# Kernel tuning notes

Measured on AMD Instinct MI355X. Metric: run time of the kernel, lower is better.

## Reference

```python
import jax, jax.numpy as jnp
import numpy as np

B, T, D, H = 2, 2048, 1024, 16
HS = D // H
EPS = 1e-5


def setup_inputs() -> dict:
    key = jax.random.key(0)
    ks = jax.random.split(key, 16)
    s = lambda *shape: 0.02
    inp = {
        "x": jax.random.normal(ks[0], (B, T, D), jnp.float32),
        # per-head Q/K/V weights stacked over heads: [H, D, HS]
        "Wq": jax.random.normal(ks[1], (H, D, HS), jnp.float32) * 0.02,
        "bq": jnp.zeros((H, HS), jnp.float32),
        "Wk": jax.random.normal(ks[2], (H, D, HS), jnp.float32) * 0.02,
        "bk": jnp.zeros((H, HS), jnp.float32),
        "Wv": jax.random.normal(ks[3], (H, D, HS), jnp.float32) * 0.02,
        "bv": jnp.zeros((H, HS), jnp.float32),
        "Wp": jax.random.normal(ks[4], (D, D), jnp.float32) * 0.02,
        "bp": jnp.zeros((D,), jnp.float32),
        "W1": jax.random.normal(ks[5], (D, 4 * D), jnp.float32) * 0.02,
        "b1": jnp.zeros((4 * D,), jnp.float32),
        "W2": jax.random.normal(ks[6], (4 * D, D), jnp.float32) * 0.02,
        "b2": jnp.zeros((D,), jnp.float32),
        "g1": jnp.ones((D,), jnp.float32),
        "be1": jnp.zeros((D,), jnp.float32),
        "g2": jnp.ones((D,), jnp.float32),
        "be2": jnp.zeros((D,), jnp.float32),
    }
    return inp


def layernorm(x, g, b):
    mu = jnp.mean(x, axis=-1, keepdims=True)
    var = jnp.mean(jnp.square(x - mu), axis=-1, keepdims=True)
    return (x - mu) * jax.lax.rsqrt(var + EPS) * g + b


def reference(x, Wq, bq, Wk, bk, Wv, bv, Wp, bp, W1, b1, W2, b2, g1, be1, g2, be2):
    # NOTE: this block applies LN then residual-adds the *normalized* x,
    # exactly as in the original (x = ln1(x); x = x + mha(x)).
    h = layernorm(x, g1, be1)
    # multi-head attention, all heads batched via stacked weights
    q = jnp.einsum('btd,hdk->bhtk', h, Wq) + bq[None, :, None, :]
    k = jnp.einsum('btd,hdk->bhtk', h, Wk) + bk[None, :, None, :]
    v = jnp.einsum('btd,hdk->bhtk', h, Wv) + bv[None, :, None, :]
    att = jnp.einsum('bhtk,bhsk->bhts', q, k) * (HS ** -0.5)  # [B,H,T,T]
    att = jax.nn.softmax(att, axis=-1)
    o = jnp.einsum('bhts,bhsk->bhtk', att, v)  # [B,H,T,HS]
    # concat heads in order along last dim -> [B,T,D]
    o = jnp.transpose(o, (0, 2, 1, 3)).reshape(B, T, D)
    o = o @ Wp + bp
    h = h + o
    h2 = layernorm(h, g2, be2)
    ff = jax.nn.gelu(h2 @ W1 + b1, approximate=False) @ W2 + b2
    return h2 + ff
```

## Files before the change

kernel.cpp:

```cpp
#include <hip/hip_runtime.h>
#include <cstdint>
#include <cstddef>

#define B_  2
#define T_  2048
#define D_  1024
#define H_  16
#define HS_ 64
#define MTOT (B_*T_)

typedef unsigned short u16;
typedef __attribute__((ext_vector_type(8))) __bf16 bf16x8;
typedef __attribute__((ext_vector_type(4))) float f32x4;

__device__ __forceinline__ u16 f2bf(float f) {
  unsigned int u = __builtin_bit_cast(unsigned int, f);
  u += 0x7fffu + ((u >> 16) & 1u);
  return (u16)(u >> 16);
}

__device__ __forceinline__ unsigned cvtpk(float lo, float hi) {
  unsigned r;
  asm("v_cvt_pk_bf16_f32 %0, %1, %2" : "=v"(r) : "v"(lo), "v"(hi));
  return r;
}

__device__ __forceinline__ void gload16(const u16* g, u16* l) {
  __builtin_amdgcn_global_load_lds((const __attribute__((address_space(1))) void*)g,
                                   (__attribute__((address_space(3))) void*)l, 16, 0, 0);
}

__global__ __launch_bounds__(256) void transpose_f2b(const float* __restrict__ in,
                                                     u16* __restrict__ out, int R, int C) {
  __shared__ float tile[32][33];
  int c0 = blockIdx.x * 32, r0 = blockIdx.y * 32;
  size_t zoff = (size_t)blockIdx.z * R * C;
  const float* src = in + zoff;
  u16* dst = out + zoff;
  int tx = threadIdx.x & 31, ty = threadIdx.x >> 5;
#pragma unroll
  for (int k = 0; k < 4; ++k)
    tile[ty + k*8][tx] = src[(size_t)(r0 + ty + k*8) * C + c0 + tx];
  __syncthreads();
#pragma unroll
  for (int k = 0; k < 4; ++k)
    dst[(size_t)(c0 + ty + k*8) * R + r0 + tx] = f2bf(tile[tx][ty + k*8]);
}

__global__ __launch_bounds__(256) void transpose_v(const u16* __restrict__ in,
                                                   u16* __restrict__ out) {
  __shared__ u16 tile[32][33];
  int z = blockIdx.z;
  int b = z >> 4, h = z & 15;
  int t0 = blockIdx.x * 32, f0 = blockIdx.y * 32;
  int tx = threadIdx.x & 31, ty = threadIdx.x >> 5;
#pragma unroll
  for (int k = 0; k < 4; ++k)
    tile[ty + k*8][tx] = in[((size_t)b*T_ + t0 + ty + k*8) * D_ + h*HS_ + f0 + tx];
  __syncthreads();
#pragma unroll
  for (int k = 0; k < 4; ++k)
    out[((size_t)z*HS_ + f0 + ty + k*8) * T_ + t0 + tx] = tile[tx][ty + k*8];
}

__global__ __launch_bounds__(256) void ln_kernel(const float* __restrict__ x,
                                                 const float* __restrict__ gg,
                                                 const float* __restrict__ be,
                                                 float* __restrict__ hf,
                                                 u16* __restrict__ hb) {
  int row = blockIdx.x;
  int t = threadIdx.x;
  const float* xr = x + (size_t)row * D_;
  float4 xv = *(const float4*)&xr[t * 4];
  float s  = xv.x + xv.y + xv.z + xv.w;
  float ss = xv.x*xv.x + xv.y*xv.y + xv.z*xv.z + xv.w*xv.w;
#pragma unroll
  for (int m = 1; m < 64; m <<= 1) { s += __shfl_xor(s, m); ss += __shfl_xor(ss, m); }
  __shared__ float red[8];
  int lane = t & 63, wv = t >> 6;
  if (lane == 0) { red[wv] = s; red[4 + wv] = ss; }
  __syncthreads();
  s  = red[0] + red[1] + red[2] + red[3];
  ss = red[4] + red[5] + red[6] + red[7];
  float mu  = s * (1.0f / D_);
  float var = ss * (1.0f / D_) - mu * mu;
  float rs  = rsqrtf(var + 1e-5f);
  float4 gv = *(const float4*)&gg[t * 4];
  float4 bv = *(const float4*)&be[t * 4];
  float4 hv;
  hv.x = (xv.x - mu) * rs * gv.x + bv.x;
  hv.y = (xv.y - mu) * rs * gv.y + bv.y;
  hv.z = (xv.z - mu) * rs * gv.z + bv.z;
  hv.w = (xv.w - mu) * rs * gv.w + bv.w;
  *(float4*)&hf[(size_t)row * D_ + t * 4] = hv;
  uint2 pk;
  pk.x = (unsigned)f2bf(hv.x) | ((unsigned)f2bf(hv.y) << 16);
  pk.y = (unsigned)f2bf(hv.z) | ((unsigned)f2bf(hv.w) << 16);
  *(uint2*)&hb[(size_t)row * D_ + t * 4] = pk;
}

template<int EPI>
__global__ __launch_bounds__(256) void gemm_bt(
    const u16* __restrict__ A, const u16* __restrict__ Bt,
    const float* __restrict__ bias0, const float* __restrict__ bias1,
    const float* __restrict__ bias2, const float* __restrict__ res,
    float* __restrict__ outf, u16* __restrict__ o0, u16* __restrict__ o1,
    u16* __restrict__ o2, int M, int N, int K, int kLen) {
  __shared__ __align__(16) u16 As[3][128 * 32];
  __shared__ __align__(16) u16 Bs[3][128 * 32];
  const int tid = threadIdx.x;
  const int lane = tid & 63, wv = tid >> 6;
  const int m0 = blockIdx.y * 128, n0 = blockIdx.x * 128;
  const int kOff = blockIdx.z * kLen;
  const int rA = lane & 15, g = lane >> 4;
  const int wm = (wv >> 1) * 64, wn = (wv & 1) * 64;
  const int sx = (rA >> 1) & 3;

  f32x4 acc[4][4] = {};

  auto stage = [&](int tt, int bufi) {
#pragma unroll
    for (int p = 0; p < 2; ++p) {
      int c = (p * 4 + wv) * 64 + lane;
      int row = c >> 2;
      int s = (c & 3) ^ ((row >> 1) & 3);
      gload16(A  + (size_t)(m0 + row) * K + kOff + tt * 32 + s * 8,
              &As[bufi][0] + (size_t)(p * 4 + wv) * 512);
      gload16(Bt + (size_t)(n0 + row) * K + kOff + tt * 32 + s * 8,
              &Bs[bufi][0] + (size_t)(p * 4 + wv) * 512);
    }
  };

  const int nk = kLen >> 5;
  stage(0, 0);
  stage(1, 1);

  int cur = 0, nxt = 2;
  for (int t = 0; t < nk; ++t) {
    if (t + 1 < nk) asm volatile("s_waitcnt vmcnt(4)" ::: "memory");
    else            asm volatile("s_waitcnt vmcnt(0)" ::: "memory");
    __builtin_amdgcn_s_barrier();
    __builtin_amdgcn_sched_barrier(0);
    if (t + 2 < nk) stage(t + 2, nxt);

    bf16x8 a[4], b[4];
#pragma unroll
    for (int i = 0; i < 4; ++i)
      a[i] = *(const bf16x8*)&As[cur][(wm + i * 16 + rA) * 32 + ((g ^ sx) << 3)];
#pragma unroll
    for (int i = 0; i < 4; ++i)
      b[i] = *(const bf16x8*)&Bs[cur][(wn + i * 16 + rA) * 32 + ((g ^ sx) << 3)];
#pragma unroll
    for (int i = 0; i < 4; ++i)
#pragma unroll
      for (int j = 0; j < 4; ++j)
        acc[i][j] = __builtin_amdgcn_mfma_f32_16x16x32_bf16(a[i], b[j], acc[i][j], 0, 0, 0);

    cur = (cur == 2) ? 0 : cur + 1;
    nxt = (nxt == 2) ? 0 : nxt + 1;
  }

#pragma unroll
  for (int i = 0; i < 4; ++i) {
#pragma unroll
    for (int j = 0; j < 4; ++j) {
#pragma unroll
      for (int r = 0; r < 4; ++r) {
        int row = m0 + wm + i * 16 + g * 4 + r;
        int col = n0 + wn + j * 16 + rA;
        float v = acc[i][j][r];
        if constexpr (EPI == 0) {
          int sel = col >> 10, nn = col & 1023;
          const float* bp = sel == 0 ? bias0 : (sel == 1 ? bias1 : bias2);
          u16* op = sel == 0 ? o0 : (sel == 1 ? o1 : o2);
          op[(size_t)row * 1024 + nn] = f2bf(v + bp[nn]);
        } else if constexpr (EPI == 1) {
          v += bias0[col];
          float z = 0.7978845608f * (v + 0.044715f * v * v * v);
          z = fminf(z, 18.0f);
          float e = __builtin_amdgcn_exp2f(z * 2.8853900817779268f);
          v = v * e / (e + 1.0f);
          o0[(size_t)row * N + col] = f2bf(v);
        } else if constexpr (EPI == 2) {
          v += bias0[col] + res[(size_t)row * N + col];
          outf[(size_t)row * N + col] = v;
        } else {
          float* dst = blockIdx.z ? (float*)o1 : outf;
          dst[(size_t)row * N + col] = v;
        }
      }
    }
  }
}

__global__ __launch_bounds__(256) void reduce_ff2(const float* __restrict__ p0,
                                                  const float* __restrict__ p1,
                                                  const float* __restrict__ bias,
                                                  const float* __restrict__ res,
                                                  float* __restrict__ out) {
  int i = (blockIdx.x * 256 + threadIdx.x) * 4;
  float4 a = *(const float4*)&p0[i];
  float4 b = *(const float4*)&p1[i];
  float4 r = *(const float4*)&res[i];
  float4 bb = *(const float4*)&bias[i & 1023];
  float4 o;
  o.x = a.x + b.x + r.x + bb.x;
  o.y = a.y + b.y + r.y + bb.y;
  o.z = a.z + b.z + r.z + bb.z;
  o.w = a.w + b.w + r.w + bb.w;
  *(float4*)&out[i] = o;
}

__global__ __launch_bounds__(256) void attn_kernel(const u16* __restrict__ qg,
                                                   const u16* __restrict__ kg,
                                                   const u16* __restrict__ vtg,
                                                   u16* __restrict__ og) {
  const int wg = blockIdx.x;
  const int qt = wg & 31;
  const int h  = (wg >> 5) & 15;
  const int b  = wg >> 9;
  const int tid = threadIdx.x, lane = tid & 63, wv = tid >> 6;
  const int q0 = qt * 64 + wv * 16;
  const int rA = lane & 15, g = lane >> 4;
  const int rx = rA & 7;

  __shared__ __align__(16) u16 Ks[2][64 * 64];
  __shared__ __align__(16) u16 Vs[2][64 * 64];
  __shared__ __align__(16) u16 Ps[4][16 * 64];

  const size_t qoff = ((size_t)b * T_ + q0 + rA) * D_ + h * HS_ + g * 8;
  const bf16x8 aq0 = *(const bf16x8*)&qg[qoff];
  const bf16x8 aq1 = *(const bf16x8*)&qg[qoff + 32];

  const u16* kbase = kg + (size_t)b * T_ * D_ + h * HS_;
  const u16* vbase = vtg + ((size_t)b * H_ + h) * HS_ * T_;

  const float cfold = 0.18033688011112042f;
  float mrun = -1e30f, lrun = 0.0f;
  f32x4 oacc[4] = {};

  auto stage = [&](int t, int buf) {
#pragma unroll
    for (int p = 0; p < 2; ++p) {
      int chunk = p * 256 + wv * 64 + lane;
      int row = chunk >> 3, s = chunk & 7;
      int ss = s ^ (row & 7);
      gload16(kbase + ((size_t)t * 64 + row) * D_ + ss * 8,
              &Ks[buf][0] + (size_t)(p * 256 + wv * 64) * 8);
      gload16(vbase + (size_t)row * T_ + t * 64 + ss * 8,
              &Vs[buf][0] + (size_t)(p * 256 + wv * 64) * 8);
    }
  };

  stage(0, 0);

  const int NT = T_ / 64;
  for (int t = 0; t < NT; ++t) {
    __syncthreads();
    const int buf = t & 1;
    if (t + 1 < NT) stage(t + 1, buf ^ 1);

    const u16* kb = &Ks[buf][0];
    f32x4 sc[4];
    __builtin_amdgcn_s_setprio(1);
#pragma unroll
    for (int st = 0; st < 4; ++st) {
      bf16x8 k0 = *(const bf16x8*)&kb[(st * 16 + rA) * 64 + ((g ^ rx) << 3)];
      bf16x8 k1 = *(const bf16x8*)&kb[(st * 16 + rA) * 64 + (((4 + g) ^ rx) << 3)];
      f32x4 z = {};
      z = __builtin_amdgcn_mfma_f32_16x16x32_bf16(k0, aq0, z, 0, 0, 0);
      z = __builtin_amdgcn_mfma_f32_16x16x32_bf16(k1, aq1, z, 0, 0, 0);
      sc[st] = z;
    }
    __builtin_amdgcn_s_setprio(0);

    float a0 = fmaxf(fmaxf(sc[0][0], sc[0][1]), fmaxf(sc[0][2], sc[0][3]));
    float a1 = fmaxf(fmaxf(sc[1][0], sc[1][1]), fmaxf(sc[1][2], sc[1][3]));
    float a2 = fmaxf(fmaxf(sc[2][0], sc[2][1]), fmaxf(sc[2][2], sc[2][3]));
    float a3 = fmaxf(fmaxf(sc[3][0], sc[3][1]), fmaxf(sc[3][2], sc[3][3]));
    float mx = fmaxf(fmaxf(a0, a1), fmaxf(a2, a3));
    mx = fmaxf(mx, __shfl_xor(mx, 16));
    mx = fmaxf(mx, __shfl_xor(mx, 32));
    float tm = mx * cfold;

    if (__any(tm > mrun + 8.0f)) {
      float mnew = fmaxf(mrun, tm);
      float sca = __builtin_amdgcn_exp2f(mrun - mnew);
      mrun = mnew;
      lrun *= sca;
#pragma unroll
      for (int f = 0; f < 4; ++f) oacc[f] *= sca;
    }

    float p[16];
#pragma unroll
    for (int st = 0; st < 4; ++st)
#pragma unroll
      for (int r = 0; r < 4; ++r)
        p[st * 4 + r] = __builtin_amdgcn_exp2f(__builtin_fmaf(sc[st][r], cfold, -mrun));

    float sum = (((p[0] + p[1]) + (p[2] + p[3])) + ((p[4] + p[5]) + (p[6] + p[7])))
              + (((p[8] + p[9]) + (p[10] + p[11])) + ((p[12] + p[13]) + (p[14] + p[15])));
    sum += __shfl_xor(sum, 16);
    sum += __shfl_xor(sum, 32);
    lrun += sum;

    char* psb = (char*)&Ps[wv][0];
#pragma unroll
    for (int st = 0; st < 4; ++st) {
      uint2 w;
      w.x = cvtpk(p[st * 4 + 0], p[st * 4 + 1]);
      w.y = cvtpk(p[st * 4 + 2], p[st * 4 + 3]);
      int slot = st * 2 + (g >> 1);
      *(uint2*)&psb[rA * 128 + (((slot ^ rx)) << 4) + ((g & 1) << 3)] = w;
    }
    bf16x8 pf0 = *(const bf16x8*)&psb[rA * 128 + ((g ^ rx) << 4)];
    bf16x8 pf1 = *(const bf16x8*)&psb[rA * 128 + (((4 + g) ^ rx) << 4)];

    const u16* vbl = &Vs[buf][0];
    __builtin_amdgcn_s_setprio(1);
#pragma unroll
    for (int f = 0; f < 4; ++f) {
      bf16x8 v0 = *(const bf16x8*)&vbl[(f * 16 + rA) * 64 + ((g ^ rx) << 3)];
      bf16x8 v1 = *(const bf16x8*)&vbl[(f * 16 + rA) * 64 + (((4 + g) ^ rx) << 3)];
      oacc[f] = __builtin_amdgcn_mfma_f32_16x16x32_bf16(v0, pf0, oacc[f], 0, 0, 0);
      oacc[f] = __builtin_amdgcn_mfma_f32_16x16x32_bf16(v1, pf1, oacc[f], 0, 0, 0);
    }
    __builtin_amdgcn_s_setprio(0);
  }

  float linv = 1.0f / lrun;
#pragma unroll
  for (int f = 0; f < 4; ++f) {
    uint2 w;
    w.x = cvtpk(oacc[f][0] * linv, oacc[f][1] * linv);
    w.y = cvtpk(oacc[f][2] * linv, oacc[f][3] * linv);
    *(uint2*)&og[((size_t)b * T_ + q0 + rA) * D_ + h * HS_ + f * 16 + g * 4] = w;
  }
}

extern "C" void kernel_launch(void* const* d_in, const int* in_sizes, int n_in,
                              void* d_out, int out_size, void* d_ws, size_t ws_size,
                              hipStream_t stream) {
  const float* x   = (const float*)d_in[0];
  const float* Wq  = (const float*)d_in[1];
  const float* bq  = (const float*)d_in[2];
  const float* Wk  = (const float*)d_in[3];
  const float* bk  = (const float*)d_in[4];
  const float* Wv  = (const float*)d_in[5];
  const float* bv  = (const float*)d_in[6];
  const float* Wp  = (const float*)d_in[7];
  const float* bp  = (const float*)d_in[8];
  const float* W1  = (const float*)d_in[9];
  const float* b1  = (const float*)d_in[10];
  const float* W2  = (const float*)d_in[11];
  const float* b2  = (const float*)d_in[12];
  const float* g1  = (const float*)d_in[13];
  const float* be1 = (const float*)d_in[14];
  const float* g2  = (const float*)d_in[15];
  const float* be2 = (const float*)d_in[16];
  float* out = (float*)d_out;

  char* w = (char*)d_ws;
  auto alloc = [&](size_t bytes) { char* p = w; w += (bytes + 255) & ~(size_t)255; return p; };
  const size_t MD = (size_t)MTOT * D_;

  float* h_f    = (float*)alloc(MD * 4);
  u16*   h_b    = (u16*)  alloc(MD * 2);
  u16*   wqkv_t = (u16*)  alloc(3 * (size_t)D_ * D_ * 2);
  u16*   wp_t   = (u16*)  alloc((size_t)D_ * D_ * 2);
  u16*   w1_t   = (u16*)  alloc((size_t)D_ * 4 * D_ * 2);
  u16*   w2_t   = (u16*)  alloc((size_t)D_ * 4 * D_ * 2);
  u16*   q_b    = (u16*)  alloc(MD * 2);
  u16*   k_b    = (u16*)  alloc(MD * 2);
  u16*   v_b    = (u16*)  alloc(MD * 2);
  u16*   vt_b   = (u16*)  alloc(MD * 2);
  u16*   o_b    = (u16*)  alloc(MD * 2);
  float* hat_f  = (float*)alloc(MD * 4);
  u16*   ff1_b  = q_b;
  float* h2_f   = h_f;
  u16*   h2_b   = h_b;
  float* pf0    = hat_f;
  float* pf1    = (float*)h_b;

  dim3 blk(256);

  transpose_f2b<<<dim3(2, 32, 16), blk, 0, stream>>>(Wq, wqkv_t, 1024, 64);
  transpose_f2b<<<dim3(2, 32, 16), blk, 0, stream>>>(Wk, wqkv_t + (size_t)D_ * D_, 1024, 64);
  transpose_f2b<<<dim3(2, 32, 16), blk, 0, stream>>>(Wv, wqkv_t + 2 * (size_t)D_ * D_, 1024, 64);
  transpose_f2b<<<dim3(32, 32, 1), blk, 0, stream>>>(Wp, wp_t, 1024, 1024);
  transpose_f2b<<<dim3(128, 32, 1), blk, 0, stream>>>(W1, w1_t, 1024, 4096);
  transpose_f2b<<<dim3(32, 128, 1), blk, 0, stream>>>(W2, w2_t, 4096, 1024);

  ln_kernel<<<dim3(MTOT), blk, 0, stream>>>(x, g1, be1, h_f, h_b);

  gemm_bt<0><<<dim3(24, 32, 1), blk, 0, stream>>>(h_b, wqkv_t, bq, bk, bv,
      nullptr, nullptr, q_b, k_b, v_b, MTOT, 3072, 1024, 1024);

  transpose_v<<<dim3(64, 2, 32), blk, 0, stream>>>(v_b, vt_b);

  attn_kernel<<<dim3(B_ * H_ * (T_ / 64)), blk, 0, stream>>>(q_b, k_b, vt_b, o_b);

  gemm_bt<2><<<dim3(8, 32, 1), blk, 0, stream>>>(o_b, wp_t, bp, nullptr, nullptr,
      h_f, hat_f, nullptr, nullptr, nullptr, MTOT, 1024, 1024, 1024);

  ln_kernel<<<dim3(MTOT), blk, 0, stream>>>(hat_f, g2, be2, h2_f, h2_b);

  gemm_bt<1><<<dim3(32, 32, 1), blk, 0, stream>>>(h2_b, w1_t, b1, nullptr, nullptr,
      nullptr, nullptr, ff1_b, nullptr, nullptr, MTOT, 4096, 1024, 1024);

  gemm_bt<3><<<dim3(8, 32, 2), blk, 0, stream>>>(ff1_b, w2_t, nullptr, nullptr,
      nullptr, nullptr, pf0, nullptr, (u16*)pf1, nullptr, MTOT, 1024, 4096, 2048);

  reduce_ff2<<<dim3(MTOT), blk, 0, stream>>>(pf0, pf1, b2, h2_f, out);
}
```

Measured before the change: 289.7 us.

## Add 256x256-tile 512-thread GEMM for QKV and FF1 projections

Measured after the change: 282.3 us. 1.03x faster.

```diff
diff --git a/kernel.cpp b/kernel.cpp
--- a/kernel.cpp
+++ b/kernel.cpp
@@ -100,12 +100,104 @@
 }
 
 template<int EPI>
+__global__ __launch_bounds__(512, 2) void gemm256(
+    const u16* __restrict__ A, const u16* __restrict__ Bt,
+    const float* __restrict__ bias0, const float* __restrict__ bias1,
+    const float* __restrict__ bias2,
+    u16* __restrict__ o0, u16* __restrict__ o1, u16* __restrict__ o2,
+    int M, int N, int K) {
+  __shared__ __align__(16) u16 As[2][256 * 64];
+  __shared__ __align__(16) u16 Bs[2][256 * 64];
+  const int tid = threadIdx.x;
+  const int lane = tid & 63, w = tid >> 6;
+  const int m0 = blockIdx.y * 256, n0 = blockIdx.x * 256;
+  const int rA = lane & 15, g = lane >> 4;
+  const int wm = (w >> 2) * 128, wn = (w & 3) * 64;
+  const int sxa = rA & 7;
+
+  f32x4 acc[8][4] = {};
+
+  auto stage = [&](int t, int bufi) {
+#pragma unroll
+    for (int i = 0; i < 4; ++i) {
+      int c = i * 512 + tid;
+      int row = c >> 3;
+      int ss = (c & 7) ^ (row & 7);
+      gload16(A + (size_t)(m0 + row) * K + t * 64 + ss * 8,
+              &As[bufi][0] + (size_t)(i * 512 + w * 64) * 8);
+    }
+#pragma unroll
+    for (int i = 0; i < 4; ++i) {
+      int c = i * 512 + tid;
+      int row = c >> 3;
+      int ss = (c & 7) ^ (row & 7);
+      gload16(Bt + (size_t)(n0 + row) * K + t * 64 + ss * 8,
+              &Bs[bufi][0] + (size_t)(i * 512 + w * 64) * 8);
+    }
+  };
+
+  stage(0, 0);
+
+  const int nk = K >> 6;
+  for (int t = 0; t < nk; ++t) {
+    __syncthreads();
+    const int buf = t & 1;
+    if (t + 1 < nk) stage(t + 1, buf ^ 1);
+
+    bf16x8 bfr[4][2];
+#pragma unroll
+    for (int j = 0; j < 4; ++j) {
+      int br = wn + j * 16 + rA;
+#pragma unroll
+      for (int kk = 0; kk < 2; ++kk)
+        bfr[j][kk] = *(const bf16x8*)&Bs[buf][br * 64 + (((kk * 4 + g) ^ sxa) << 3)];
+    }
+#pragma unroll
+    for (int i = 0; i < 8; ++i) {
+      int ar = wm + i * 16 + rA;
+      bf16x8 a0 = *(const bf16x8*)&As[buf][ar * 64 + ((g ^ sxa) << 3)];
+      bf16x8 a1 = *(const bf16x8*)&As[buf][ar * 64 + (((4 + g) ^ sxa) << 3)];
+#pragma unroll
+      for (int j = 0; j < 4; ++j) {
+        acc[i][j] = __builtin_amdgcn_mfma_f32_16x16x32_bf16(a0, bfr[j][0], acc[i][j], 0, 0, 0);
+        acc[i][j] = __builtin_amdgcn_mfma_f32_16x16x32_bf16(a1, bfr[j][1], acc[i][j], 0, 0, 0);
+      }
+    }
+  }
+
+#pragma unroll
+  for (int i = 0; i < 8; ++i) {
+#pragma unroll
+    for (int j = 0; j < 4; ++j) {
+#pragma unroll
+      for (int r = 0; r < 4; ++r) {
+        int row = m0 + wm + i * 16 + g * 4 + r;
+        int col = n0 + wn + j * 16 + rA;
+        float v = acc[i][j][r];
+        if constexpr (EPI == 0) {
+          int sel = col >> 10, nn = col & 1023;
+          const float* bp = sel == 0 ? bias0 : (sel == 1 ? bias1 : bias2);
+          u16* op = sel == 0 ? o0 : (sel == 1 ? o1 : o2);
+          op[(size_t)row * 1024 + nn] = f2bf(v + bp[nn]);
+        } else {
+          v += bias0[col];
+          float z = 0.7978845608f * (v + 0.044715f * v * v * v);
+          z = fminf(z, 18.0f);
+          float e = __builtin_amdgcn_exp2f(z * 2.8853900817779268f);
+          v = v * e / (e + 1.0f);
+          o0[(size_t)row * N + col] = f2bf(v);
+        }
+      }
+    }
+  }
+}
+
+template<int EPI>
 __global__ __launch_bounds__(256) void gemm_bt(
     const u16* __restrict__ A, const u16* __restrict__ Bt,
-    const float* __restrict__ bias0, const float* __restrict__ bias1,
-    const float* __restrict__ bias2, const float* __restrict__ res,
-    float* __restrict__ outf, u16* __restrict__ o0, u16* __restrict__ o1,
-    u16* __restrict__ o2, int M, int N, int K, int kLen) {
+    const float* __restrict__ bias0, const float* __restrict__ res,
+    float* __restrict__ outf, float* __restrict__ p1,
+    int M, int N, int K, int kLen) {
   __shared__ __align__(16) u16 As[3][128 * 32];
   __shared__ __align__(16) u16 Bs[3][128 * 32];
   const int tid = threadIdx.x;
@@ -169,23 +261,11 @@
         int row = m0 + wm + i * 16 + g * 4 + r;
         int col = n0 + wn + j * 16 + rA;
         float v = acc[i][j][r];
-        if constexpr (EPI == 0) {
-          int sel = col >> 10, nn = col & 1023;
-          const float* bp = sel == 0 ? bias0 : (sel == 1 ? bias1 : bias2);
-          u16* op = sel == 0 ? o0 : (sel == 1 ? o1 : o2);
-          op[(size_t)row * 1024 + nn] = f2bf(v + bp[nn]);
-        } else if constexpr (EPI == 1) {
-          v += bias0[col];
-          float z = 0.7978845608f * (v + 0.044715f * v * v * v);
-          z = fminf(z, 18.0f);
-          float e = __builtin_amdgcn_exp2f(z * 2.8853900817779268f);
-          v = v * e / (e + 1.0f);
-          o0[(size_t)row * N + col] = f2bf(v);
-        } else if constexpr (EPI == 2) {
+        if constexpr (EPI == 2) {
           v += bias0[col] + res[(size_t)row * N + col];
           outf[(size_t)row * N + col] = v;
         } else {
-          float* dst = blockIdx.z ? (float*)o1 : outf;
+          float* dst = blockIdx.z ? p1 : outf;
           dst[(size_t)row * N + col] = v;
         }
       }
@@ -394,23 +474,23 @@
 
   ln_kernel<<<dim3(MTOT), blk, 0, stream>>>(x, g1, be1, h_f, h_b);
 
-  gemm_bt<0><<<dim3(24, 32, 1), blk, 0, stream>>>(h_b, wqkv_t, bq, bk, bv,
-      nullptr, nullptr, q_b, k_b, v_b, MTOT, 3072, 1024, 1024);
+  gemm256<0><<<dim3(12, 16), dim3(512), 0, stream>>>(h_b, wqkv_t, bq, bk, bv,
+      q_b, k_b, v_b, MTOT, 3072, 1024);
 
   transpose_v<<<dim3(64, 2, 32), blk, 0, stream>>>(v_b, vt_b);
 
   attn_kernel<<<dim3(B_ * H_ * (T_ / 64)), blk, 0, stream>>>(q_b, k_b, vt_b, o_b);
 
-  gemm_bt<2><<<dim3(8, 32, 1), blk, 0, stream>>>(o_b, wp_t, bp, nullptr, nullptr,
-      h_f, hat_f, nullptr, nullptr, nullptr, MTOT, 1024, 1024, 1024);
+  gemm_bt<2><<<dim3(8, 32, 1), blk, 0, stream>>>(o_b, wp_t, bp, h_f, hat_f,
+      nullptr, MTOT, 1024, 1024, 1024);
 
   ln_kernel<<<dim3(MTOT), blk, 0, stream>>>(hat_f, g2, be2, h2_f, h2_b);
 
-  gemm_bt<1><<<dim3(32, 32, 1), blk, 0, stream>>>(h2_b, w1_t, b1, nullptr, nullptr,
-      nullptr, nullptr, ff1_b, nullptr, nullptr, MTOT, 4096, 1024, 1024);
+  gemm256<1><<<dim3(16, 16), dim3(512), 0, stream>>>(h2_b, w1_t, b1, nullptr, nullptr,
+      ff1_b, nullptr, nullptr, MTOT, 4096, 1024);
 
   gemm_bt<3><<<dim3(8, 32, 2), blk, 0, stream>>>(ff1_b, w2_t, nullptr, nullptr,
-      nullptr, nullptr, pf0, nullptr, (u16*)pf1, nullptr, MTOT, 1024, 4096, 2048);
+      pf0, pf1, MTOT, 1024, 4096, 2048);
 
   reduce_ff2<<<dim3(MTOT), blk, 0, stream>>>(pf0, pf1, b2, h2_f, out);
 }
```
